# Performance work log

Hardware: AMD Instinct MI355X
Metric: run time of the kernel (lower is better)

The kernel has to match this reference:

```python
import jax, jax.numpy as jnp
import numpy as np

B, N, M, D = 32, 1024, 1024, 256


def setup_inputs() -> dict:
    key = jax.random.key(0)
    k1, k2, k3, k4 = jax.random.split(key, 4)
    h1 = jax.random.normal(k1, (B, N, D), dtype=jnp.float32)
    h2 = jax.random.normal(k2, (B, M, D), dtype=jnp.float32)
    W = jax.random.normal(k3, (D,), dtype=jnp.float32) * (1.0 / np.sqrt(D))
    b = jax.random.normal(k4, (1,), dtype=jnp.float32) * (1.0 / np.sqrt(D))
    return {"h1": h1, "h2": h2, "W": W, "b": b}


def reference(h1, h2, W, b):
    # Pairwise squared L2 distance (p=2, abs(x-y)^2 == (x-y)^2), halved as in the
    # original: dist_matrix = cdist(g1, g2) / 2.0. Use the ||x||^2+||y||^2-2xy
    # expansion to avoid materializing the [B,N,M,D] difference tensor.
    sq1 = jnp.sum(h1 * h1, axis=-1)                      # [B, N]
    sq2 = jnp.sum(h2 * h2, axis=-1)                      # [B, M]
    cross = jnp.einsum('bnd,bmd->bnm', h1, h2)           # [B, N, M]
    dist = jnp.maximum(sq1[:, :, None] + sq2[:, None, :] - 2.0 * cross, 0.0) * 0.5

    # Insertion/deletion cost: |Linear(h)| per node.
    d1 = jnp.abs(jnp.einsum('bnd,d->bn', h1, W) + b)     # [B, N]
    d2 = jnp.abs(jnp.einsum('bmd,d->bm', h2, W) + b)     # [B, M]

    a = jnp.minimum(jnp.min(dist, axis=1), d2)           # min over rows -> [B, M]
    bb = jnp.minimum(jnp.min(dist, axis=2), d1)          # min over cols -> [B, N]
    d = jnp.mean(a, axis=-1) + jnp.mean(bb, axis=-1)     # [B]
    return d
```

## Files before the change

kernel.cpp:

```cpp
#include <hip/hip_runtime.h>


#define B_  32
#define N_  1024
#define M_  1024
#define D_  256
#define BN_ (B_ * N_)

#define TILE 128
#define BK   32

typedef short bf16x8 __attribute__((ext_vector_type(8)));
typedef float f32x4  __attribute__((ext_vector_type(4)));

__device__ __forceinline__ short f2bf(float x) {
  unsigned u = __float_as_uint(x);
  u += 0x7fffu + ((u >> 16) & 1u);
  return (short)(u >> 16);
}


__global__ __launch_bounds__(256) void dist_kernel(
    const float* __restrict__ h1, const float* __restrict__ h2,
    const float* __restrict__ W, const float* __restrict__ bias,
    float* __restrict__ ws) {
  __shared__ __align__(16) unsigned short Abuf[2][TILE * BK];
  __shared__ __align__(16) unsigned short Bbuf[2][TILE * BK];
  __shared__ float sqrow[TILE], sqcol[TILE];
  __shared__ float rowred[TILE][2], colred[TILE][2];

  const int bid = blockIdx.x;
  const int b   = ((bid >> 9) << 3) + (bid & 7);
  const int t6  = (bid >> 3) & 63;
  const int bm  = t6 & 7;
  const int bn  = t6 >> 3;

  const int tid  = threadIdx.x;
  const int lane = tid & 63;
  const int wid  = tid >> 6;
  const int wr   = wid >> 1, wc = wid & 1;

  const int srow = tid >> 1, sh = tid & 1;

  const float4* pA = (const float4*)(h1 + (size_t)(b * N_ + bn * TILE + srow) * D_ + sh * 16);
  const float4* pB = (const float4*)(h2 + (size_t)(b * M_ + bm * TILE + srow) * D_ + sh * 16);
  const float4* pW = (const float4*)(W + sh * 16);

  char* const abase = (char*)Abuf;
  char* const bbase = (char*)Bbuf;
  const int wsw = (srow * 64 + sh * 32) ^ ((srow & 7) << 4);

  const int arow = wr * 64 + (lane & 15);
  const int brow = wc * 64 + (lane & 15);
  const int aoff = (arow * 64 + ((lane >> 4) * 16)) ^ ((arow & 7) << 4);
  const int boff = (brow * 64 + ((lane >> 4) * 16)) ^ ((brow & 7) << 4);

  const bool needW = (bm == 0) || (bn == 0);

  f32x4 acc[4][4];
#pragma unroll
  for (int i = 0; i < 4; ++i)
#pragma unroll
    for (int j = 0; j < 4; ++j) acc[i][j] = (f32x4){0.f, 0.f, 0.f, 0.f};

  float sqA = 0.f, sqB = 0.f, dwA = 0.f, dwB = 0.f;
  float4 La[4], Lb[4], Lw[4];

  auto ldnext = [&]() {
#pragma unroll
    for (int i = 0; i < 4; ++i) { La[i] = pA[i]; Lb[i] = pB[i]; }
    if (needW) {
#pragma unroll
      for (int i = 0; i < 4; ++i) Lw[i] = pW[i];
    }
    pA += 8; pB += 8; pW += 8;
  };

  auto stage = [&](int c) {
#pragma unroll
    for (int i = 0; i < 4; ++i) {
      sqA = fmaf(La[i].x, La[i].x, sqA); sqA = fmaf(La[i].y, La[i].y, sqA);
      sqA = fmaf(La[i].z, La[i].z, sqA); sqA = fmaf(La[i].w, La[i].w, sqA);
      sqB = fmaf(Lb[i].x, Lb[i].x, sqB); sqB = fmaf(Lb[i].y, Lb[i].y, sqB);
      sqB = fmaf(Lb[i].z, Lb[i].z, sqB); sqB = fmaf(Lb[i].w, Lb[i].w, sqB);
    }
    if (bm == 0) {
#pragma unroll
      for (int i = 0; i < 4; ++i) {
        dwA = fmaf(La[i].x, Lw[i].x, dwA); dwA = fmaf(La[i].y, Lw[i].y, dwA);
        dwA = fmaf(La[i].z, Lw[i].z, dwA); dwA = fmaf(La[i].w, Lw[i].w, dwA);
      }
    }
    if (bn == 0) {
#pragma unroll
      for (int i = 0; i < 4; ++i) {
        dwB = fmaf(Lb[i].x, Lw[i].x, dwB); dwB = fmaf(Lb[i].y, Lw[i].y, dwB);
        dwB = fmaf(Lb[i].z, Lw[i].z, dwB); dwB = fmaf(Lb[i].w, Lw[i].w, dwB);
      }
    }
    const bf16x8 va0 = {f2bf(La[0].x), f2bf(La[0].y), f2bf(La[0].z), f2bf(La[0].w),
                        f2bf(La[1].x), f2bf(La[1].y), f2bf(La[1].z), f2bf(La[1].w)};
    const bf16x8 va1 = {f2bf(La[2].x), f2bf(La[2].y), f2bf(La[2].z), f2bf(La[2].w),
                        f2bf(La[3].x), f2bf(La[3].y), f2bf(La[3].z), f2bf(La[3].w)};
    const bf16x8 vb0 = {f2bf(Lb[0].x), f2bf(Lb[0].y), f2bf(Lb[0].z), f2bf(Lb[0].w),
                        f2bf(Lb[1].x), f2bf(Lb[1].y), f2bf(Lb[1].z), f2bf(Lb[1].w)};
    const bf16x8 vb1 = {f2bf(Lb[2].x), f2bf(Lb[2].y), f2bf(Lb[2].z), f2bf(Lb[2].w),
                        f2bf(Lb[3].x), f2bf(Lb[3].y), f2bf(Lb[3].z), f2bf(Lb[3].w)};
    *(bf16x8*)(abase + c * 8192 + wsw)        = va0;
    *(bf16x8*)(abase + c * 8192 + (wsw ^ 16)) = va1;
    *(bf16x8*)(bbase + c * 8192 + wsw)        = vb0;
    *(bf16x8*)(bbase + c * 8192 + (wsw ^ 16)) = vb1;
  };

  auto domfma = [&](int c) {
    const char* ab = abase + c * 8192;
    const char* bb = bbase + c * 8192;
    bf16x8 af[4], bfv[4];
#pragma unroll
    for (int mi = 0; mi < 4; ++mi) af[mi]  = *(const bf16x8*)(ab + aoff + mi * 1024);
#pragma unroll
    for (int nj = 0; nj < 4; ++nj) bfv[nj] = *(const bf16x8*)(bb + boff + nj * 1024);
#pragma unroll
    for (int mi = 0; mi < 4; ++mi)
#pragma unroll
      for (int nj = 0; nj < 4; ++nj)
        acc[mi][nj] = __builtin_amdgcn_mfma_f32_16x16x32_bf16(af[mi], bfv[nj], acc[mi][nj], 0, 0, 0);
  };

  ldnext();
  stage(0);
  __syncthreads();
  int cur = 0;
#pragma unroll 1
  for (int t = 0; t < 7; ++t) {
    ldnext();
    domfma(cur);
    stage(cur ^ 1);
    __syncthreads();
    cur ^= 1;
  }
  domfma(cur);

  const float sqAf = sqA + __shfl_xor(sqA, 1);
  const float sqBf = sqB + __shfl_xor(sqB, 1);
  const float dwAf = dwA + __shfl_xor(dwA, 1);
  const float dwBf = dwB + __shfl_xor(dwB, 1);
  if ((tid & 1) == 0) {
    sqrow[srow] = sqAf;
    sqcol[srow] = sqBf;
    const float b0 = bias[0];
    if (bm == 0) ws[b * N_ + bn * TILE + srow]       = fabsf(dwAf + b0);
    if (bn == 0) ws[BN_ + b * M_ + bm * TILE + srow] = fabsf(dwBf + b0);
  }
  __syncthreads();

  float sj[4];
#pragma unroll
  for (int nj = 0; nj < 4; ++nj) sj[nj] = sqcol[wc * 64 + nj * 16 + (lane & 15)];

  float rminv[4][4];
  float cminv[4] = {3.0e38f, 3.0e38f, 3.0e38f, 3.0e38f};
#pragma unroll
  for (int mi = 0; mi < 4; ++mi)
#pragma unroll
    for (int r = 0; r < 4; ++r) {
      const float si = sqrow[wr * 64 + mi * 16 + (lane >> 4) * 4 + r];
      float rm = 3.0e38f;
#pragma unroll
      for (int nj = 0; nj < 4; ++nj) {
        const float dd = fmaxf(fmaf(-2.f, acc[mi][nj][r], si + sj[nj]), 0.f) * 0.5f;
        rm = fminf(rm, dd);
        cminv[nj] = fminf(cminv[nj], dd);
      }
      rminv[mi][r] = rm;
    }

#pragma unroll
  for (int mi = 0; mi < 4; ++mi)
#pragma unroll
    for (int r = 0; r < 4; ++r) {
      float v = rminv[mi][r];
      v = fminf(v, __shfl_xor(v, 1));
      v = fminf(v, __shfl_xor(v, 2));
      v = fminf(v, __shfl_xor(v, 4));
      v = fminf(v, __shfl_xor(v, 8));
      rminv[mi][r] = v;
    }
  if ((lane & 15) == 0) {
#pragma unroll
    for (int mi = 0; mi < 4; ++mi)
#pragma unroll
      for (int r = 0; r < 4; ++r)
        rowred[wr * 64 + mi * 16 + (lane >> 4) * 4 + r][wc] = rminv[mi][r];
  }

#pragma unroll
  for (int nj = 0; nj < 4; ++nj) {
    float v = cminv[nj];
    v = fminf(v, __shfl_xor(v, 16));
    v = fminf(v, __shfl_xor(v, 32));
    cminv[nj] = v;
  }
  if (lane < 16) {
#pragma unroll
    for (int nj = 0; nj < 4; ++nj)
      colred[wc * 64 + nj * 16 + lane][wr] = cminv[nj];
  }
  __syncthreads();

  unsigned* rming = (unsigned*)(ws + 2 * BN_);
  unsigned* cming = (unsigned*)(ws + 3 * BN_);
  if (tid < TILE) {
    const float v = fminf(rowred[tid][0], rowred[tid][1]);
    atomicMin(&rming[b * N_ + bn * TILE + tid], __float_as_uint(v));
  } else {
    const int c = tid - TILE;
    const float v = fminf(colred[c][0], colred[c][1]);
    atomicMin(&cming[b * M_ + bm * TILE + c], __float_as_uint(v));
  }
}

__global__ __launch_bounds__(256) void finish_kernel(
    const float* __restrict__ ws, float* __restrict__ out) {
  const int b = blockIdx.x;
  const int tid = threadIdx.x;
  const float* dd1  = ws + b * N_;
  const float* dd2  = ws + BN_ + b * M_;
  const float* rmin = ws + 2 * BN_ + b * N_;
  const float* cmin = ws + 3 * BN_ + b * M_;

  float s = 0.f;
  for (int i = tid; i < N_; i += 256)
    s += fminf(rmin[i], dd1[i]) + fminf(cmin[i], dd2[i]);

  __shared__ float sm[4];
  for (int off = 32; off; off >>= 1) s += __shfl_down(s, off);
  if ((tid & 63) == 0) sm[tid >> 6] = s;
  __syncthreads();
  if (tid == 0) out[b] = (sm[0] + sm[1] + sm[2] + sm[3]) * (1.f / 1024.f);
}

extern "C" void kernel_launch(void* const* d_in, const int* in_sizes, int n_in,
                              void* d_out, int out_size, void* d_ws, size_t ws_size,
                              hipStream_t stream) {
  (void)in_sizes; (void)n_in; (void)out_size; (void)ws_size;
  const float* h1   = (const float*)d_in[0];
  const float* h2   = (const float*)d_in[1];
  const float* W    = (const float*)d_in[2];
  const float* bias = (const float*)d_in[3];
  float* ws  = (float*)d_ws;
  float* out = (float*)d_out;

  hipMemsetAsync(ws + 2 * BN_, 0x7F, (size_t)2 * BN_ * sizeof(float), stream);

  dist_kernel<<<dim3(2048), 256, 0, stream>>>(h1, h2, W, bias, ws);
  finish_kernel<<<B_, 256, 0, stream>>>(ws, out);
}
```

Before: 146.6 us.

## Precompute bf16 operands and norms in a prep kernel, load tiles directly to LDS

A new prep kernel converts h1 and h2 to bf16 once per row. In the same pass it computes the squared norms and the |Wx+b| costs, and it initializes the atomic-min buffers, which replaces the memset. The GEMM kernel then streams half-width bf16 tiles straight into LDS with global_load_lds. This removes the repeated fp32 reads and conversions each tile used to do. The cost is an extra launch and a single-buffered LDS loop with two barriers per k-step. When workspace is too small, it falls back to writing bf16 into the input buffers in place.

```diff
diff --git a/kernel.cpp b/kernel.cpp
--- a/kernel.cpp
+++ b/kernel.cpp
@@ -3,29 +3,63 @@
 
 #define B_  32
 #define N_  1024
-#define M_  1024
 #define D_  256
 #define BN_ (B_ * N_)
-
 #define TILE 128
 #define BK   32
 
 typedef short bf16x8 __attribute__((ext_vector_type(8)));
 typedef float f32x4  __attribute__((ext_vector_type(4)));
-
-__device__ __forceinline__ short f2bf(float x) {
-  unsigned u = __float_as_uint(x);
+typedef unsigned short u16;
+typedef unsigned int   u32;
+
+__device__ __forceinline__ u16 f2bf(float x) {
+  u32 u = __float_as_uint(x);
   u += 0x7fffu + ((u >> 16) & 1u);
-  return (short)(u >> 16);
-}
-
-
-__global__ __launch_bounds__(256) void dist_kernel(
+  return (u16)(u >> 16);
+}
+
+__device__ __forceinline__ void gload16(const void* g, void* l) {
+  __builtin_amdgcn_global_load_lds((const __attribute__((address_space(1))) u32*)g,
+                                   (__attribute__((address_space(3))) u32*)l, 16, 0, 0);
+}
+
+
+__global__ __launch_bounds__(256) void prep_kernel(
     const float* __restrict__ h1, const float* __restrict__ h2,
     const float* __restrict__ W, const float* __restrict__ bias,
-    float* __restrict__ ws) {
-  __shared__ __align__(16) unsigned short Abuf[2][TILE * BK];
-  __shared__ __align__(16) unsigned short Bbuf[2][TILE * BK];
+    u16* __restrict__ bfA, u16* __restrict__ bfB, int strideSh,
+    float* __restrict__ fl) {
+  const int tid = threadIdx.x, lane = tid & 63, wid = tid >> 6;
+  const int gw  = blockIdx.x * 4 + wid;
+  const int isB = gw >> 15;
+  const int row = gw & 32767;
+
+  const float4 v = *(const float4*)((isB ? h2 : h1) + (size_t)row * D_ + lane * 4);
+  const float4 w = *(const float4*)(W + lane * 4);
+  float sq = v.x * v.x + v.y * v.y + v.z * v.z + v.w * v.w;
+  float dw = v.x * w.x + v.y * w.y + v.z * w.z + v.w * w.w;
+#pragma unroll
+  for (int off = 1; off < 64; off <<= 1) {
+    sq += __shfl_xor(sq, off);
+    dw += __shfl_xor(dw, off);
+  }
+
+  const ushort4 o = {f2bf(v.x), f2bf(v.y), f2bf(v.z), f2bf(v.w)};
+  *(ushort4*)((isB ? bfB : bfA) + (size_t)row * strideSh + lane * 4) = o;
+
+  if (lane == 0) {
+    fl[isB * BN_ + row]       = fabsf(dw + bias[0]);
+    fl[(2 + isB) * BN_ + row] = sq;
+  }
+  if (lane == 1) ((u32*)fl)[(4 + isB) * BN_ + row] = 0x7f7f7f7fu;
+}
+
+__global__ __launch_bounds__(256) void gemm_kernel(
+    const u16* __restrict__ bfA, const u16* __restrict__ bfB, int strideSh,
+    float* __restrict__ fl) {
+  __shared__ __align__(16) u16 As[TILE * BK];
+  __shared__ __align__(16) u16 Bs[TILE * BK];
   __shared__ float sqrow[TILE], sqcol[TILE];
   __shared__ float rowred[TILE][2], colred[TILE][2];
 
@@ -35,86 +69,45 @@
   const int bm  = t6 & 7;
   const int bn  = t6 >> 3;
 
-  const int tid  = threadIdx.x;
-  const int lane = tid & 63;
-  const int wid  = tid >> 6;
-  const int wr   = wid >> 1, wc = wid & 1;
-
-  const int srow = tid >> 1, sh = tid & 1;
-
-  const float4* pA = (const float4*)(h1 + (size_t)(b * N_ + bn * TILE + srow) * D_ + sh * 16);
-  const float4* pB = (const float4*)(h2 + (size_t)(b * M_ + bm * TILE + srow) * D_ + sh * 16);
-  const float4* pW = (const float4*)(W + sh * 16);
-
-  char* const abase = (char*)Abuf;
-  char* const bbase = (char*)Bbuf;
-  const int wsw = (srow * 64 + sh * 32) ^ ((srow & 7) << 4);
+  const int tid = threadIdx.x, lane = tid & 63, wid = tid >> 6;
+  const int wr = wid >> 1, wc = wid & 1;
+
+  if (tid < TILE) sqrow[tid] = fl[2 * BN_ + b * N_ + bn * TILE + tid];
+  else            sqcol[tid - TILE] = fl[3 * BN_ + b * N_ + bm * TILE + (tid - TILE)];
+
+  const char* srcA[2]; const char* srcB[2];
+#pragma unroll
+  for (int c = 0; c < 2; ++c) {
+    const int o   = (wid * 2 + c) * 1024 + lane * 16;
+    const int lin = o ^ (((o >> 6) & 7) << 4);
+    const int row = lin >> 6;
+    const int kb  = lin & 63;
+    srcA[c] = (const char*)(bfA + (size_t)(b * N_ + bn * TILE + row) * strideSh) + kb;
+    srcB[c] = (const char*)(bfB + (size_t)(b * N_ + bm * TILE + row) * strideSh) + kb;
+  }
+
+  f32x4 acc[4][4];
+#pragma unroll
+  for (int i = 0; i < 4; ++i)
+#pragma unroll
+    for (int j = 0; j < 4; ++j) acc[i][j] = (f32x4){0.f, 0.f, 0.f, 0.f};
 
   const int arow = wr * 64 + (lane & 15);
   const int brow = wc * 64 + (lane & 15);
   const int aoff = (arow * 64 + ((lane >> 4) * 16)) ^ ((arow & 7) << 4);
   const int boff = (brow * 64 + ((lane >> 4) * 16)) ^ ((brow & 7) << 4);
-
-  const bool needW = (bm == 0) || (bn == 0);
-
-  f32x4 acc[4][4];
-#pragma unroll
-  for (int i = 0; i < 4; ++i)
-#pragma unroll
-    for (int j = 0; j < 4; ++j) acc[i][j] = (f32x4){0.f, 0.f, 0.f, 0.f};
-
-  float sqA = 0.f, sqB = 0.f, dwA = 0.f, dwB = 0.f;
-  float4 La[4], Lb[4], Lw[4];
-
-  auto ldnext = [&]() {
-#pragma unroll
-    for (int i = 0; i < 4; ++i) { La[i] = pA[i]; Lb[i] = pB[i]; }
-    if (needW) {
-#pragma unroll
-      for (int i = 0; i < 4; ++i) Lw[i] = pW[i];
+  const char* ab = (const char*)As;
+  const char* bb = (const char*)Bs;
+
+#pragma unroll 1
+  for (int ks = 0; ks < 8; ++ks) {
+#pragma unroll
+    for (int c = 0; c < 2; ++c) {
+      gload16(srcA[c], &As[(wid * 2 + c) * 512]);
+      gload16(srcB[c], &Bs[(wid * 2 + c) * 512]);
+      srcA[c] += 64; srcB[c] += 64;
     }
-    pA += 8; pB += 8; pW += 8;
-  };
-
-  auto stage = [&](int c) {
-#pragma unroll
-    for (int i = 0; i < 4; ++i) {
-      sqA = fmaf(La[i].x, La[i].x, sqA); sqA = fmaf(La[i].y, La[i].y, sqA);
-      sqA = fmaf(La[i].z, La[i].z, sqA); sqA = fmaf(La[i].w, La[i].w, sqA);
-      sqB = fmaf(Lb[i].x, Lb[i].x, sqB); sqB = fmaf(Lb[i].y, Lb[i].y, sqB);
-      sqB = fmaf(Lb[i].z, Lb[i].z, sqB); sqB = fmaf(Lb[i].w, Lb[i].w, sqB);
-    }
-    if (bm == 0) {
-#pragma unroll
-      for (int i = 0; i < 4; ++i) {
-        dwA = fmaf(La[i].x, Lw[i].x, dwA); dwA = fmaf(La[i].y, Lw[i].y, dwA);
-        dwA = fmaf(La[i].z, Lw[i].z, dwA); dwA = fmaf(La[i].w, Lw[i].w, dwA);
-      }
-    }
-    if (bn == 0) {
-#pragma unroll
-      for (int i = 0; i < 4; ++i) {
-        dwB = fmaf(Lb[i].x, Lw[i].x, dwB); dwB = fmaf(Lb[i].y, Lw[i].y, dwB);
-        dwB = fmaf(Lb[i].z, Lw[i].z, dwB); dwB = fmaf(Lb[i].w, Lw[i].w, dwB);
-      }
-    }
-    const bf16x8 va0 = {f2bf(La[0].x), f2bf(La[0].y), f2bf(La[0].z), f2bf(La[0].w),
-                        f2bf(La[1].x), f2bf(La[1].y), f2bf(La[1].z), f2bf(La[1].w)};
-    const bf16x8 va1 = {f2bf(La[2].x), f2bf(La[2].y), f2bf(La[2].z), f2bf(La[2].w),
-                        f2bf(La[3].x), f2bf(La[3].y), f2bf(La[3].z), f2bf(La[3].w)};
-    const bf16x8 vb0 = {f2bf(Lb[0].x), f2bf(Lb[0].y), f2bf(Lb[0].z), f2bf(Lb[0].w),
-                        f2bf(Lb[1].x), f2bf(Lb[1].y), f2bf(Lb[1].z), f2bf(Lb[1].w)};
-    const bf16x8 vb1 = {f2bf(Lb[2].x), f2bf(Lb[2].y), f2bf(Lb[2].z), f2bf(Lb[2].w),
-                        f2bf(Lb[3].x), f2bf(Lb[3].y), f2bf(Lb[3].z), f2bf(Lb[3].w)};
-    *(bf16x8*)(abase + c * 8192 + wsw)        = va0;
-    *(bf16x8*)(abase + c * 8192 + (wsw ^ 16)) = va1;
-    *(bf16x8*)(bbase + c * 8192 + wsw)        = vb0;
-    *(bf16x8*)(bbase + c * 8192 + (wsw ^ 16)) = vb1;
-  };
-
-  auto domfma = [&](int c) {
-    const char* ab = abase + c * 8192;
-    const char* bb = bbase + c * 8192;
+    __syncthreads();
     bf16x8 af[4], bfv[4];
 #pragma unroll
     for (int mi = 0; mi < 4; ++mi) af[mi]  = *(const bf16x8*)(ab + aoff + mi * 1024);
@@ -125,34 +118,8 @@
 #pragma unroll
       for (int nj = 0; nj < 4; ++nj)
         acc[mi][nj] = __builtin_amdgcn_mfma_f32_16x16x32_bf16(af[mi], bfv[nj], acc[mi][nj], 0, 0, 0);
-  };
-
-  ldnext();
-  stage(0);
-  __syncthreads();
-  int cur = 0;
-#pragma unroll 1
-  for (int t = 0; t < 7; ++t) {
-    ldnext();
-    domfma(cur);
-    stage(cur ^ 1);
     __syncthreads();
-    cur ^= 1;
-  }
-  domfma(cur);
-
-  const float sqAf = sqA + __shfl_xor(sqA, 1);
-  const float sqBf = sqB + __shfl_xor(sqB, 1);
-  const float dwAf = dwA + __shfl_xor(dwA, 1);
-  const float dwBf = dwB + __shfl_xor(dwB, 1);
-  if ((tid & 1) == 0) {
-    sqrow[srow] = sqAf;
-    sqcol[srow] = sqBf;
-    const float b0 = bias[0];
-    if (bm == 0) ws[b * N_ + bn * TILE + srow]       = fabsf(dwAf + b0);
-    if (bn == 0) ws[BN_ + b * M_ + bm * TILE + srow] = fabsf(dwBf + b0);
-  }
-  __syncthreads();
+  }
 
   float sj[4];
 #pragma unroll
@@ -208,26 +175,26 @@
   }
   __syncthreads();
 
-  unsigned* rming = (unsigned*)(ws + 2 * BN_);
-  unsigned* cming = (unsigned*)(ws + 3 * BN_);
+  u32* rming = (u32*)(fl + 4 * BN_);
+  u32* cming = (u32*)(fl + 5 * BN_);
   if (tid < TILE) {
     const float v = fminf(rowred[tid][0], rowred[tid][1]);
     atomicMin(&rming[b * N_ + bn * TILE + tid], __float_as_uint(v));
   } else {
     const int c = tid - TILE;
     const float v = fminf(colred[c][0], colred[c][1]);
-    atomicMin(&cming[b * M_ + bm * TILE + c], __float_as_uint(v));
+    atomicMin(&cming[b * N_ + bm * TILE + c], __float_as_uint(v));
   }
 }
 
 __global__ __launch_bounds__(256) void finish_kernel(
-    const float* __restrict__ ws, float* __restrict__ out) {
+    const float* __restrict__ fl, float* __restrict__ out) {
   const int b = blockIdx.x;
   const int tid = threadIdx.x;
-  const float* dd1  = ws + b * N_;
-  const float* dd2  = ws + BN_ + b * M_;
-  const float* rmin = ws + 2 * BN_ + b * N_;
-  const float* cmin = ws + 3 * BN_ + b * M_;
+  const float* dd1  = fl + b * N_;
+  const float* dd2  = fl + BN_ + b * N_;
+  const float* rmin = fl + 4 * BN_ + b * N_;
+  const float* cmin = fl + 5 * BN_ + b * N_;
 
   float s = 0.f;
   for (int i = tid; i < N_; i += 256)
@@ -243,16 +210,30 @@
 extern "C" void kernel_launch(void* const* d_in, const int* in_sizes, int n_in,
                               void* d_out, int out_size, void* d_ws, size_t ws_size,
                               hipStream_t stream) {
-  (void)in_sizes; (void)n_in; (void)out_size; (void)ws_size;
+  (void)in_sizes; (void)n_in; (void)out_size;
   const float* h1   = (const float*)d_in[0];
   const float* h2   = (const float*)d_in[1];
   const float* W    = (const float*)d_in[2];
   const float* bias = (const float*)d_in[3];
-  float* ws  = (float*)d_ws;
   float* out = (float*)d_out;
 
-  hipMemsetAsync(ws + 2 * BN_, 0x7F, (size_t)2 * BN_ * sizeof(float), stream);
-
-  dist_kernel<<<dim3(2048), 256, 0, stream>>>(h1, h2, W, bias, ws);
-  finish_kernel<<<B_, 256, 0, stream>>>(ws, out);
-}
+  const size_t BF_BYTES = (size_t)BN_ * D_ * 2;
+  const size_t NEED     = 2 * BF_BYTES + 6u * BN_ * 4;
+
+  u16 *bfA, *bfB; int strideSh; float* fl;
+  if (ws_size >= NEED) {
+    bfA = (u16*)d_ws;
+    bfB = (u16*)((char*)d_ws + BF_BYTES);
+    strideSh = D_;
+    fl = (float*)((char*)d_ws + 2 * BF_BYTES);
+  } else {
+    bfA = (u16*)d_in[0];
+    bfB = (u16*)d_in[1];
+    strideSh = 2 * D_;
+    fl = (float*)d_ws;
+  }
+
+  prep_kernel<<<dim3(16384), 256, 0, stream>>>(h1, h2, W, bias, bfA, bfB, strideSh, fl);
+  gemm_kernel<<<dim3(2048), 256, 0, stream>>>(bfA, bfB, strideSh, fl);
+  finish_kernel<<<dim3(B_), 256, 0, stream>>>(fl, out);
+}
```

After: 144.5 us. No clear change (-1.5%).
